# Kernel optimization log

Measured on AMD Instinct MI355X. Metric: run time of the kernel, lower is better.

The kernel has to match this reference:

```python
import jax, jax.numpy as jnp
import numpy as np

N_NODES = 100000
NEG_SLOPE = 0.2


def gat_conv(x, edge_index, W, a_src, a_dst, bias):
    """PyG GATConv, heads=1, concat, add_self_loops=True."""
    N = x.shape[0]
    loop = jnp.arange(N, dtype=edge_index.dtype)
    src = jnp.concatenate([edge_index[0], loop])  # message sources j
    dst = jnp.concatenate([edge_index[1], loop])  # message targets i
    h = x @ W                                      # [N, out]
    asrc = h @ a_src                               # [N]
    adst = h @ a_dst                               # [N]
    e = jax.nn.leaky_relu(asrc[src] + adst[dst], NEG_SLOPE)   # [E+N]
    m = jax.ops.segment_max(e, dst, num_segments=N)           # per-dst max
    w = jnp.exp(e - jax.lax.stop_gradient(m)[dst])
    denom = jax.ops.segment_sum(w, dst, num_segments=N)
    alpha = w / denom[dst]                                     # softmax per dst
    out = jax.ops.segment_sum(alpha[:, None] * h[src], dst, num_segments=N)
    return out + bias


def setup_inputs() -> dict:
    key = jax.random.key(0)
    ks = jax.random.split(key, 16)
    N, E, D = N_NODES, 3200000, 128
    x = jax.random.normal(ks[0], (N, D), dtype=jnp.float32)
    edge_index = jax.random.randint(ks[1], (2, E), 0, N, dtype=jnp.int64)
    def glorot(k, shape):
        fan = sum(shape)
        return jax.random.uniform(k, shape, jnp.float32, -1.0, 1.0) * np.sqrt(6.0 / fan)
    return {
        "x": x,
        "edge_index": edge_index,
        "W1": glorot(ks[2], (D, 16)),
        "a1_src": glorot(ks[3], (16,)),
        "a1_dst": glorot(ks[4], (16,)),
        "b1": jnp.zeros((16,), jnp.float32),
        "W2": glorot(ks[5], (16, 10)),
        "a2_src": glorot(ks[6], (10,)),
        "a2_dst": glorot(ks[7], (10,)),
        "b2": jnp.zeros((10,), jnp.float32),
        "Wl1": glorot(ks[8], (10, 10)),
        "bl1": jnp.zeros((10,), jnp.float32),
        "Wl2": glorot(ks[9], (10, 1)),
        "bl2": jnp.zeros((1,), jnp.float32),
    }


def reference(x, edge_index, W1, a1_src, a1_dst, b1, W2, a2_src, a2_dst, b2,
              Wl1, bl1, Wl2, bl2):
    h = gat_conv(x, edge_index, W1, a1_src, a1_dst, b1)
    h = jax.nn.relu(h)
    h = gat_conv(h, edge_index, W2, a2_src, a2_dst, b2)
    h = h @ Wl1 + bl1
    h = jax.nn.relu(h)
    return h @ Wl2 + bl2  # [N, 1]
```

## Files before the change

### kernel.cpp

```cpp
#include <hip/hip_runtime.h>
#include <hip/hip_fp16.h>


#define NEG 0.2f
#define FSH 7
#define BNODES 128
#define NSBMAX 1024
#define CAPB 4608
#define TILE 4096
#define PES 9

__device__ __forceinline__ float lrelu(float x) { return x > 0.0f ? x : NEG * x; }

__device__ __forceinline__ unsigned fenc(float f) {
    unsigned u = __float_as_uint(f);
    return (u & 0x80000000u) ? ~u : (u | 0x80000000u);
}
__device__ __forceinline__ float fdec(unsigned e) {
    return (e & 0x80000000u) ? __uint_as_float(e & 0x7FFFFFFFu) : __uint_as_float(~e);
}

__device__ __forceinline__ float4 ldh4(const __half* h, size_t off) {
    uint2 u = *(const uint2*)(h + off);
    __half2 a = *(__half2*)&u.x, b = *(__half2*)&u.y;
    float2 fa = __half22float2(a), fb = __half22float2(b);
    return make_float4(fa.x, fa.y, fb.x, fb.y);
}

__global__ __launch_bounds__(256) void k_front(
    const float* __restrict__ x, const float* __restrict__ W1,
    const float* __restrict__ a1s, const float* __restrict__ a1d,
    __half* __restrict__ h1, float* __restrict__ s1, float* __restrict__ d1,
    unsigned* __restrict__ gmax,
    const int* __restrict__ esrc, const int* __restrict__ edst,
    int* __restrict__ bcur, unsigned* __restrict__ pairs,
    int N, int E, int NG, int NC, int NSB)
{
    __shared__ float smem[10500];
    int tid = threadIdx.x;
    int bid = blockIdx.x;
    long long T = (long long)NG + NC;
    int before = (int)(((long long)bid * NC) / T);
    int isc = (int)((((long long)bid + 1) * NC) / T) > before;

    if (isc) {
        unsigned* lsrt = (unsigned*)smem;
        int* lhist = (int*)smem + TILE;
        int* lofs  = lhist + NSBMAX;
        int* gbase = lofs + NSBMAX;
        int* wsum  = gbase + NSBMAX;
        int cid = before;
        int base = cid * TILE;
        int tcnt = min(TILE, E - base);
        for (int i = tid; i < NSB; i += 256) lhist[i] = 0;
        __syncthreads();
        for (int i = tid; i < tcnt; i += 256)
            atomicAdd(&lhist[edst[base + i] >> FSH], 1);
        __syncthreads();
        int i0 = 4 * tid;
        int a0 = (i0 + 0 < NSB) ? lhist[i0 + 0] : 0;
        int a1 = (i0 + 1 < NSB) ? lhist[i0 + 1] : 0;
        int a2 = (i0 + 2 < NSB) ? lhist[i0 + 2] : 0;
        int a3 = (i0 + 3 < NSB) ? lhist[i0 + 3] : 0;
        int s = a0 + a1 + a2 + a3, pfx = s;
#pragma unroll
        for (int off = 1; off < 64; off <<= 1) {
            int t = __shfl_up(pfx, off, 64);
            if ((tid & 63) >= off) pfx += t;
        }
        if ((tid & 63) == 63) wsum[tid >> 6] = pfx;
        __syncthreads();
        int carry = 0;
        for (int w = 0; w < (tid >> 6); ++w) carry += wsum[w];
        int excl = pfx + carry - s;
        if (i0 + 0 < NSB) { lofs[i0 + 0] = excl;                 gbase[i0 + 0] = a0 ? atomicAdd(&bcur[(i0 + 0) * 16], a0) : 0; }
        if (i0 + 1 < NSB) { lofs[i0 + 1] = excl + a0;            gbase[i0 + 1] = a1 ? atomicAdd(&bcur[(i0 + 1) * 16], a1) : 0; }
        if (i0 + 2 < NSB) { lofs[i0 + 2] = excl + a0 + a1;       gbase[i0 + 2] = a2 ? atomicAdd(&bcur[(i0 + 2) * 16], a2) : 0; }
        if (i0 + 3 < NSB) { lofs[i0 + 3] = excl + a0 + a1 + a2;  gbase[i0 + 3] = a3 ? atomicAdd(&bcur[(i0 + 3) * 16], a3) : 0; }
        __syncthreads();
        if (i0 + 0 < NSB) lhist[i0 + 0] = lofs[i0 + 0];
        if (i0 + 1 < NSB) lhist[i0 + 1] = lofs[i0 + 1];
        if (i0 + 2 < NSB) lhist[i0 + 2] = lofs[i0 + 2];
        if (i0 + 3 < NSB) lhist[i0 + 3] = lofs[i0 + 3];
        __syncthreads();
        for (int i = tid; i < tcnt; i += 256) {
            int e = base + i;
            int d = edst[e], srcv = esrc[e];
            int pos = atomicAdd(&lhist[d >> FSH], 1);
            lsrt[pos] = ((unsigned)(d & (BNODES - 1)) << 17) | (unsigned)srcv;
        }
        __syncthreads();
        for (int i = tid; i < tcnt; i += 256) {
            int lo = 0, hi = NSB - 1;
            while (lo < hi) { int mid = (lo + hi + 1) >> 1; if (lofs[mid] <= i) lo = mid; else hi = mid - 1; }
            int rel = gbase[lo] + (i - lofs[lo]);
            if (rel < CAPB) pairs[(size_t)lo * CAPB + rel] = lsrt[i];
        }
        return;
    }

    float* sW = smem;
    float* sx = smem + 2048;
    float* wm = smem + 2048 + 64 * 132;
    int gid = bid - before;
    for (int i = tid; i < 2048; i += 256) sW[i] = W1[i];
    int node0 = gid * 64;
    for (int i = tid; i < 64 * 32; i += 256) {
        int row = i >> 5, c4 = i & 31;
        int n = node0 + row;
        float4 v = make_float4(0.f, 0.f, 0.f, 0.f);
        if (n < N) v = ((const float4*)x)[(size_t)n * 32 + c4];
        *(float4*)&sx[row * 132 + c4 * 4] = v;
    }
    __syncthreads();

    int node = node0 + (tid >> 2);
    int grp  = tid & 3;
    const float* xr = &sx[(tid >> 2) * 132];
    float4 acc = make_float4(0.f, 0.f, 0.f, 0.f);
#pragma unroll 8
    for (int j = 0; j < 128; ++j) {
        float xv = xr[j];
        float4 w = *(const float4*)&sW[j * 16 + grp * 4];
        acc.x += xv * w.x; acc.y += xv * w.y; acc.z += xv * w.z; acc.w += xv * w.w;
    }
    float4 as = ((const float4*)a1s)[grp];
    float4 ad = ((const float4*)a1d)[grp];
    float sv = acc.x * as.x + acc.y * as.y + acc.z * as.z + acc.w * as.w;
    float dv = acc.x * ad.x + acc.y * ad.y + acc.z * ad.z + acc.w * ad.w;
    sv += __shfl_xor(sv, 1); sv += __shfl_xor(sv, 2);
    dv += __shfl_xor(dv, 1); dv += __shfl_xor(dv, 2);
    if (node < N) {
        __half2 p0 = __floats2half2_rn(acc.x, acc.y);
        __half2 p1 = __floats2half2_rn(acc.z, acc.w);
        uint2 u; u.x = *(unsigned*)&p0; u.y = *(unsigned*)&p1;
        *(uint2*)&h1[(size_t)node * 16 + grp * 4] = u;
        if (grp == 0) { s1[node] = sv; d1[node] = dv; }
    }
    float m = (node < N) ? sv : -3.4e38f;
#pragma unroll
    for (int off = 32; off >= 1; off >>= 1) m = fmaxf(m, __shfl_xor(m, off));
    if ((tid & 63) == 0) wm[tid >> 6] = m;
    __syncthreads();
    if (tid == 0) {
        float b = fmaxf(fmaxf(wm[0], wm[1]), fmaxf(wm[2], wm[3]));
        atomicMax(gmax, fenc(b));
    }
}

__global__ __launch_bounds__(512) void k_agg1(
    const int* __restrict__ bcur, const unsigned* __restrict__ pairs,
    const int* __restrict__ esrc, const int* __restrict__ edst,
    const float* __restrict__ s1, const float* __restrict__ d1, const __half* __restrict__ h1,
    const float* __restrict__ b1, const float* __restrict__ W2,
    const float* __restrict__ a2s, const float* __restrict__ a2d,
    __half* __restrict__ h2, float* __restrict__ s2, float* __restrict__ d2,
    const unsigned* __restrict__ gmax1p, unsigned* __restrict__ gmax2, int N, int E)
{
    __shared__ unsigned srt[CAPB];
    __shared__ float accs[BNODES * 17];
    __shared__ int lcnt[BNODES];
    __shared__ int lofs[BNODES + 1];
    __shared__ float dds[BNODES], mbs[BNODES];
    __shared__ float sW[160], sb[16], sas[16], sad[16];
    __shared__ int wsum[8];
    __shared__ float wm[8];

    int tid = threadIdx.x;
    int fb = blockIdx.x;
    if (tid < 160) sW[tid] = W2[tid];
    if (tid < 16) {
        sb[tid]  = b1[tid];
        sas[tid] = (tid < 10) ? a2s[tid] : 0.f;
        sad[tid] = (tid < 10) ? a2d[tid] : 0.f;
    }
    int node0 = fb << FSH;
    float g0 = fdec(*gmax1p);
    if (tid < BNODES) {
        int n = node0 + tid;
        float dd = (n < N) ? d1[n] : 0.f;
        dds[tid] = dd; mbs[tid] = lrelu(g0 + dd);
        lcnt[tid] = 0;
    }
    __syncthreads();

    int rbase = fb * CAPB;
    int cnt = bcur[fb * 16];
    int gg = tid >> 2, q = tid & 3;

    if (cnt <= CAPB) {
        unsigned pe[PES];
#pragma unroll
        for (int u = 0; u < PES; ++u) {
            int i = tid + u * 512;
            bool ok = (i < cnt);
            pe[u] = ok ? pairs[rbase + i] : 0u;
            if (ok) atomicAdd(&lcnt[(pe[u] >> 17) & (BNODES - 1)], 1);
        }
        __syncthreads();
        int c = (tid < BNODES) ? lcnt[tid] : 0;
        int pfx = c;
#pragma unroll
        for (int off = 1; off < 64; off <<= 1) {
            int t = __shfl_up(pfx, off, 64);
            if ((tid & 63) >= off) pfx += t;
        }
        if ((tid & 63) == 63) wsum[tid >> 6] = pfx;
        __syncthreads();
        int carry = 0;
        for (int w = 0; w < (tid >> 6); ++w) carry += wsum[w];
        pfx += carry;
        if (tid < BNODES) { lofs[tid + 1] = pfx; lcnt[tid] = pfx - c; }
        if (tid == 0) lofs[0] = 0;
        __syncthreads();
#pragma unroll
        for (int u = 0; u < PES; ++u) {
            int i = tid + u * 512;
            if (i < cnt) {
                unsigned p = pe[u];
                int pos = atomicAdd(&lcnt[(p >> 17) & (BNODES - 1)], 1);
                srt[pos] = p & 0x1FFFF;
            }
        }
        __syncthreads();

        int n = node0 + gg;
        float4 accv; float den;
        if (n < N) {
            float w = __expf(lrelu(s1[n] + dds[gg]) - mbs[gg]);
            float4 hv = ldh4(h1, (size_t)n * 16 + 4 * q);
            accv = make_float4(w * hv.x, w * hv.y, w * hv.z, w * hv.w);
            den = w;
        } else { accv = make_float4(0.f, 0.f, 0.f, 0.f); den = 0.f; }
        {
            float dd = dds[gg], mb = mbs[gg];
            int j = lofs[gg], j1 = lofs[gg + 1];
            for (; j + 4 <= j1; j += 4) {
                int e0 = srt[j], e1 = srt[j + 1], e2 = srt[j + 2], e3 = srt[j + 3];
                float4 H0 = ldh4(h1, (size_t)e0 * 16 + 4 * q);
                float4 H1 = ldh4(h1, (size_t)e1 * 16 + 4 * q);
                float4 H2 = ldh4(h1, (size_t)e2 * 16 + 4 * q);
                float4 H3 = ldh4(h1, (size_t)e3 * 16 + 4 * q);
                int eq = srt[j + q];
                float wq = __expf(lrelu(s1[eq] + dd) - mb);
                float w0 = __shfl(wq, 0, 4), w1 = __shfl(wq, 1, 4);
                float w2 = __shfl(wq, 2, 4), w3 = __shfl(wq, 3, 4);
                accv.x += w0 * H0.x + w1 * H1.x + w2 * H2.x + w3 * H3.x;
                accv.y += w0 * H0.y + w1 * H1.y + w2 * H2.y + w3 * H3.y;
                accv.z += w0 * H0.z + w1 * H1.z + w2 * H2.z + w3 * H3.z;
                accv.w += w0 * H0.w + w1 * H1.w + w2 * H2.w + w3 * H3.w;
                den += (w0 + w1) + (w2 + w3);
            }
            for (; j < j1; ++j) {
                int e0 = srt[j];
                float w0 = __expf(lrelu(s1[e0] + dd) - mb);
                float4 H0 = ldh4(h1, (size_t)e0 * 16 + 4 * q);
                accv.x += w0 * H0.x; accv.y += w0 * H0.y;
                accv.z += w0 * H0.z; accv.w += w0 * H0.w;
                den += w0;
            }
        }
        accs[gg * 17 + 4 * q + 0] = accv.x;
        accs[gg * 17 + 4 * q + 1] = accv.y;
        accs[gg * 17 + 4 * q + 2] = accv.z;
        accs[gg * 17 + 4 * q + 3] = accv.w;
        if (q == 0) accs[gg * 17 + 16] = den;
        __syncthreads();
    } else {
        for (int i = tid; i < BNODES * 17; i += 512) accs[i] = 0.f;
        __syncthreads();
        if (tid < BNODES) {
            int n = node0 + tid;
            if (n < N) {
                float w = __expf(lrelu(s1[n] + dds[tid]) - mbs[tid]);
#pragma unroll
                for (int t = 0; t < 16; ++t)
                    accs[tid * 17 + t] = w * __half2float(h1[(size_t)n * 16 + t]);
                accs[tid * 17 + 16] = w;
            }
        }
        __syncthreads();
        for (int i = tid; i < E; i += 512) {
            int d = edst[i];
            if ((d >> FSH) != fb) continue;
            int nl = d & (BNODES - 1), src = esrc[i];
            float w = __expf(lrelu(s1[src] + dds[nl]) - mbs[nl]);
#pragma unroll
            for (int t = 0; t < 16; ++t)
                atomicAdd(&accs[nl * 17 + t], w * __half2float(h1[(size_t)src * 16 + t]));
            atomicAdd(&accs[nl * 17 + 16], w);
        }
        __syncthreads();
    }

    int g = tid >> 4, k = tid & 15;
    float sval = -3.4e38f;
#pragma unroll
    for (int qq = 0; qq < 4; ++qq) {
        int nl = g * 4 + qq, nn = node0 + nl;
        if (nn >= N) continue;
        float inv = 1.f / accs[nl * 17 + 16];
        float o = fmaxf(accs[nl * 17 + k] * inv + sb[k], 0.f);
        float hh = 0.f;
#pragma unroll
        for (int kk = 0; kk < 16; ++kk) {
            float ov = __shfl(o, kk, 16);
            if (k < 10) hh += ov * sW[kk * 10 + k];
        }
        if (k >= 10) hh = 0.f;
        float ts = hh * sas[k];
        float td = hh * sad[k];
#pragma unroll
        for (int off = 1; off < 16; off <<= 1) {
            ts += __shfl_xor(ts, off, 16);
            td += __shfl_xor(td, off, 16);
        }
        h2[(size_t)nn * 16 + k] = __float2half_rn(hh);
        if (k == 0) { s2[nn] = ts; d2[nn] = td; }
        sval = fmaxf(sval, ts);
    }
    float m = sval;
#pragma unroll
    for (int off = 32; off >= 1; off >>= 1) m = fmaxf(m, __shfl_xor(m, off));
    if ((tid & 63) == 0) wm[tid >> 6] = m;
    __syncthreads();
    if (tid == 0) {
        float bmx = wm[0];
#pragma unroll
        for (int i = 1; i < 8; ++i) bmx = fmaxf(bmx, wm[i]);
        atomicMax(gmax2, fenc(bmx));
    }
}

__global__ __launch_bounds__(512) void k_agg2(
    const int* __restrict__ bcur, const unsigned* __restrict__ pairs,
    const int* __restrict__ esrc, const int* __restrict__ edst,
    const float* __restrict__ s2, const float* __restrict__ d2, const __half* __restrict__ h2,
    const float* __restrict__ b2, const float* __restrict__ Wl1, const float* __restrict__ bl1,
    const float* __restrict__ Wl2, const float* __restrict__ bl2,
    const unsigned* __restrict__ gmax2p, float* __restrict__ out, int N, int E)
{
    __shared__ unsigned srt[CAPB];
    __shared__ float accs[BNODES * 17];
    __shared__ int lcnt[BNODES];
    __shared__ int lofs[BNODES + 1];
    __shared__ float dds[BNODES], mbs[BNODES];
    __shared__ float sW1[100], sb1[16], sW2[16], sb2g[16];
    __shared__ float sbl2;
    __shared__ int wsum[8];

    int tid = threadIdx.x;
    int fb = blockIdx.x;
    if (tid < 100) sW1[tid] = Wl1[tid];
    if (tid < 16) {
        sb1[tid]  = (tid < 10) ? bl1[tid] : 0.f;
        sW2[tid]  = (tid < 10) ? Wl2[tid] : 0.f;
        sb2g[tid] = (tid < 10) ? b2[tid]  : 0.f;
    }
    if (tid == 0) sbl2 = bl2[0];
    int node0 = fb << FSH;
    float g0 = fdec(*gmax2p);
    if (tid < BNODES) {
        int n = node0 + tid;
        float dd = (n < N) ? d2[n] : 0.f;
        dds[tid] = dd; mbs[tid] = lrelu(g0 + dd);
        lcnt[tid] = 0;
    }
    __syncthreads();

    int rbase = fb * CAPB;
    int cnt = bcur[fb * 16];
    int gg = tid >> 2, q = tid & 3;

    if (cnt <= CAPB) {
        unsigned pe[PES];
#pragma unroll
        for (int u = 0; u < PES; ++u) {
            int i = tid + u * 512;
            bool ok = (i < cnt);
            pe[u] = ok ? pairs[rbase + i] : 0u;
            if (ok) atomicAdd(&lcnt[(pe[u] >> 17) & (BNODES - 1)], 1);
        }
        __syncthreads();
        int c = (tid < BNODES) ? lcnt[tid] : 0;
        int pfx = c;
#pragma unroll
        for (int off = 1; off < 64; off <<= 1) {
            int t = __shfl_up(pfx, off, 64);
            if ((tid & 63) >= off) pfx += t;
        }
        if ((tid & 63) == 63) wsum[tid >> 6] = pfx;
        __syncthreads();
        int carry = 0;
        for (int w = 0; w < (tid >> 6); ++w) carry += wsum[w];
        pfx += carry;
        if (tid < BNODES) { lofs[tid + 1] = pfx; lcnt[tid] = pfx - c; }
        if (tid == 0) lofs[0] = 0;
        __syncthreads();
#pragma unroll
        for (int u = 0; u < PES; ++u) {
            int i = tid + u * 512;
            if (i < cnt) {
                unsigned p = pe[u];
                int pos = atomicAdd(&lcnt[(p >> 17) & (BNODES - 1)], 1);
                srt[pos] = p & 0x1FFFF;
            }
        }
        __syncthreads();

        int n = node0 + gg;
        float4 accv; float den;
        if (n < N) {
            float w = __expf(lrelu(s2[n] + dds[gg]) - mbs[gg]);
            float4 hv = ldh4(h2, (size_t)n * 16 + 4 * q);
            accv = make_float4(w * hv.x, w * hv.y, w * hv.z, w * hv.w);
            den = w;
        } else { accv = make_float4(0.f, 0.f, 0.f, 0.f); den = 0.f; }
        {
            float dd = dds[gg], mb = mbs[gg];
            int j = lofs[gg], j1 = lofs[gg + 1];
            for (; j + 4 <= j1; j += 4) {
                int e0 = srt[j], e1 = srt[j + 1], e2 = srt[j + 2], e3 = srt[j + 3];
                float4 H0 = ldh4(h2, (size_t)e0 * 16 + 4 * q);
                float4 H1 = ldh4(h2, (size_t)e1 * 16 + 4 * q);
                float4 H2 = ldh4(h2, (size_t)e2 * 16 + 4 * q);
                float4 H3 = ldh4(h2, (size_t)e3 * 16 + 4 * q);
                int eq = srt[j + q];
                float wq = __expf(lrelu(s2[eq] + dd) - mb);
                float w0 = __shfl(wq, 0, 4), w1 = __shfl(wq, 1, 4);
                float w2 = __shfl(wq, 2, 4), w3 = __shfl(wq, 3, 4);
                accv.x += w0 * H0.x + w1 * H1.x + w2 * H2.x + w3 * H3.x;
                accv.y += w0 * H0.y + w1 * H1.y + w2 * H2.y + w3 * H3.y;
                accv.z += w0 * H0.z + w1 * H1.z + w2 * H2.z + w3 * H3.z;
                accv.w += w0 * H0.w + w1 * H1.w + w2 * H2.w + w3 * H3.w;
                den += (w0 + w1) + (w2 + w3);
            }
            for (; j < j1; ++j) {
                int e0 = srt[j];
                float w0 = __expf(lrelu(s2[e0] + dd) - mb);
                float4 H0 = ldh4(h2, (size_t)e0 * 16 + 4 * q);
                accv.x += w0 * H0.x; accv.y += w0 * H0.y;
                accv.z += w0 * H0.z; accv.w += w0 * H0.w;
                den += w0;
            }
        }
        accs[gg * 17 + 4 * q + 0] = accv.x;
        accs[gg * 17 + 4 * q + 1] = accv.y;
        accs[gg * 17 + 4 * q + 2] = accv.z;
        accs[gg * 17 + 4 * q + 3] = accv.w;
        if (q == 0) accs[gg * 17 + 16] = den;
        __syncthreads();
    } else {
        for (int i = tid; i < BNODES * 17; i += 512) accs[i] = 0.f;
        __syncthreads();
        if (tid < BNODES) {
            int n = node0 + tid;
            if (n < N) {
                float w = __expf(lrelu(s2[n] + dds[tid]) - mbs[tid]);
#pragma unroll
                for (int t = 0; t < 16; ++t)
                    accs[tid * 17 + t] = w * __half2float(h2[(size_t)n * 16 + t]);
                accs[tid * 17 + 16] = w;
            }
        }
        __syncthreads();
        for (int i = tid; i < E; i += 512) {
            int d = edst[i];
            if ((d >> FSH) != fb) continue;
            int nl = d & (BNODES - 1), src = esrc[i];
            float w = __expf(lrelu(s2[src] + dds[nl]) - mbs[nl]);
#pragma unroll
            for (int t = 0; t < 16; ++t)
                atomicAdd(&accs[nl * 17 + t], w * __half2float(h2[(size_t)src * 16 + t]));
            atomicAdd(&accs[nl * 17 + 16], w);
        }
        __syncthreads();
    }

    int g = tid >> 4, k = tid & 15;
    bool fk = k < 10;
#pragma unroll
    for (int qq = 0; qq < 4; ++qq) {
        int nl = g * 4 + qq, nn = node0 + nl;
        if (nn >= N) continue;
        float inv = 1.f / accs[nl * 17 + 16];
        float o = fk ? accs[nl * 17 + k] * inv + sb2g[k] : 0.f;
        float v = sb1[k];
#pragma unroll
        for (int kk = 0; kk < 10; ++kk) {
            float ov = __shfl(o, kk, 16);
            if (fk) v += ov * sW1[kk * 10 + k];
        }
        float t = fmaxf(v, 0.f);
        float cc = t * sW2[k];
#pragma unroll
        for (int off = 1; off < 16; off <<= 1) cc += __shfl_xor(cc, off, 16);
        if (k == 0) out[nn] = cc + sbl2;
    }
}

extern "C" void kernel_launch(void* const* d_in, const int* in_sizes, int n_in,
                              void* d_out, int out_size, void* d_ws, size_t ws_size,
                              hipStream_t stream)
{
    const float* x   = (const float*)d_in[0];
    const int*   ei  = (const int*)  d_in[1];
    const float* W1  = (const float*)d_in[2];
    const float* a1s = (const float*)d_in[3];
    const float* a1d = (const float*)d_in[4];
    const float* b1  = (const float*)d_in[5];
    const float* W2  = (const float*)d_in[6];
    const float* a2s = (const float*)d_in[7];
    const float* a2d = (const float*)d_in[8];
    const float* b2  = (const float*)d_in[9];
    const float* Wl1 = (const float*)d_in[10];
    const float* bl1 = (const float*)d_in[11];
    const float* Wl2 = (const float*)d_in[12];
    const float* bl2 = (const float*)d_in[13];

    int N = in_sizes[0] / 128;
    int E = in_sizes[1] / 2;
    const int* ei_src = ei;
    const int* ei_dst = ei + E;
    int NSB = (N + BNODES - 1) >> FSH;

    size_t Np = ((size_t)N + 3) & ~(size_t)3;
    size_t need_bytes = (16 + (size_t)NSB * 16) * 4 + Np * 20 * 4 + (size_t)NSB * CAPB * 4;
    if (ws_size < need_bytes) return;

    unsigned* gmax1 = (unsigned*)d_ws;
    unsigned* gmax2 = gmax1 + 1;
    int* bcur = (int*)d_ws + 16;
    float* rest = (float*)d_ws + 16 + (size_t)NSB * 16;
    __half* h1 = (__half*)rest;
    float* s1 = rest + Np * 8;
    float* d1 = s1 + Np;
    __half* h2 = (__half*)(d1 + Np);
    float* s2 = (float*)(h2) + Np * 8;
    float* d2 = s2 + Np;
    unsigned* pairs = (unsigned*)(d2 + Np);

    int NG = (N + 63) / 64;
    int NC = (E + TILE - 1) / TILE;

    hipMemsetAsync(d_ws, 0, (16 + (size_t)NSB * 16) * sizeof(int), stream);
    hipLaunchKernelGGL(k_front, dim3(NG + NC), dim3(256), 0, stream,
                       x, W1, a1s, a1d, h1, s1, d1, gmax1,
                       ei_src, ei_dst, bcur, pairs, N, E, NG, NC, NSB);
    hipLaunchKernelGGL(k_agg1, dim3(NSB), dim3(512), 0, stream,
                       bcur, pairs, ei_src, ei_dst, s1, d1, h1, b1, W2, a2s, a2d,
                       h2, s2, d2, gmax1, gmax2, N, E);
    hipLaunchKernelGGL(k_agg2, dim3(NSB), dim3(512), 0, stream,
                       bcur, pairs, ei_src, ei_dst, s2, d2, h2, b2, Wl1, bl1, Wl2, bl2,
                       gmax2, (float*)d_out, N, E);
}
```

Before: 279.1 us.

## Split per-node edge lists across lane pairs with 16-byte feature gathers

The four lanes per destination node are regrouped into two pairs. Each pair handles half of the node's edge list, and each lane gathers 8 half-precision features with one 16-byte load instead of 4 with an 8-byte load. The partial sums are combined with xor shuffles. Separately, the edge tile size in the front kernel is doubled, which enlarges its shared memory buffer. The aim is fewer, wider gather instructions and more parallelism within each node's edge list. The cost is extra shuffle reductions, more registers per lane, and more shared memory in the front kernel.

```diff
diff --git a/kernel.cpp b/kernel.cpp
--- a/kernel.cpp
+++ b/kernel.cpp
@@ -7,7 +7,7 @@
 #define BNODES 128
 #define NSBMAX 1024
 #define CAPB 4608
-#define TILE 4096
+#define TILE 8192
 #define PES 9
 
 __device__ __forceinline__ float lrelu(float x) { return x > 0.0f ? x : NEG * x; }
@@ -25,6 +25,16 @@
     __half2 a = *(__half2*)&u.x, b = *(__half2*)&u.y;
     float2 fa = __half22float2(a), fb = __half22float2(b);
     return make_float4(fa.x, fa.y, fb.x, fb.y);
+}
+
+__device__ __forceinline__ void ldh8(const __half* h, size_t off, float4& a, float4& b) {
+    uint4 u = *(const uint4*)(h + off);
+    __half2 p0 = *(__half2*)&u.x, p1 = *(__half2*)&u.y;
+    __half2 p2 = *(__half2*)&u.z, p3 = *(__half2*)&u.w;
+    float2 f0 = __half22float2(p0), f1 = __half22float2(p1);
+    float2 f2 = __half22float2(p2), f3 = __half22float2(p3);
+    a = make_float4(f0.x, f0.y, f1.x, f1.y);
+    b = make_float4(f2.x, f2.y, f3.x, f3.y);
 }
 
 __global__ __launch_bounds__(256) void k_front(
@@ -36,7 +46,7 @@
     int* __restrict__ bcur, unsigned* __restrict__ pairs,
     int N, int E, int NG, int NC, int NSB)
 {
-    __shared__ float smem[10500];
+    __shared__ float smem[11268];
     int tid = threadIdx.x;
     int bid = blockIdx.x;
     long long T = (long long)NG + NC;
@@ -225,46 +235,67 @@
         __syncthreads();
 
         int n = node0 + gg;
-        float4 accv; float den;
-        if (n < N) {
-            float w = __expf(lrelu(s1[n] + dds[gg]) - mbs[gg]);
-            float4 hv = ldh4(h1, (size_t)n * 16 + 4 * q);
-            accv = make_float4(w * hv.x, w * hv.y, w * hv.z, w * hv.w);
+        int sub = q >> 1, ql = q & 1;
+        float dd = dds[gg], mb = mbs[gg];
+        float4 aA = make_float4(0.f, 0.f, 0.f, 0.f);
+        float4 aB = make_float4(0.f, 0.f, 0.f, 0.f);
+        float den = 0.f;
+        if (n < N && sub == 0) {
+            float w = __expf(lrelu(s1[n] + dd) - mb);
+            float4 hA, hB; ldh8(h1, (size_t)n * 16 + 8 * ql, hA, hB);
+            aA = make_float4(w * hA.x, w * hA.y, w * hA.z, w * hA.w);
+            aB = make_float4(w * hB.x, w * hB.y, w * hB.z, w * hB.w);
             den = w;
-        } else { accv = make_float4(0.f, 0.f, 0.f, 0.f); den = 0.f; }
+        }
         {
-            float dd = dds[gg], mb = mbs[gg];
-            int j = lofs[gg], j1 = lofs[gg + 1];
+            int lo = lofs[gg], hi = lofs[gg + 1];
+            int half = (hi - lo + 1) >> 1;
+            int j  = lo + sub * half;
+            int j1 = sub ? hi : lo + half;
             for (; j + 4 <= j1; j += 4) {
                 int e0 = srt[j], e1 = srt[j + 1], e2 = srt[j + 2], e3 = srt[j + 3];
-                float4 H0 = ldh4(h1, (size_t)e0 * 16 + 4 * q);
-                float4 H1 = ldh4(h1, (size_t)e1 * 16 + 4 * q);
-                float4 H2 = ldh4(h1, (size_t)e2 * 16 + 4 * q);
-                float4 H3 = ldh4(h1, (size_t)e3 * 16 + 4 * q);
-                int eq = srt[j + q];
-                float wq = __expf(lrelu(s1[eq] + dd) - mb);
-                float w0 = __shfl(wq, 0, 4), w1 = __shfl(wq, 1, 4);
-                float w2 = __shfl(wq, 2, 4), w3 = __shfl(wq, 3, 4);
-                accv.x += w0 * H0.x + w1 * H1.x + w2 * H2.x + w3 * H3.x;
-                accv.y += w0 * H0.y + w1 * H1.y + w2 * H2.y + w3 * H3.y;
-                accv.z += w0 * H0.z + w1 * H1.z + w2 * H2.z + w3 * H3.z;
-                accv.w += w0 * H0.w + w1 * H1.w + w2 * H2.w + w3 * H3.w;
+                int eA = ql ? e1 : e0, eB = ql ? e3 : e2;
+                float wqA = __expf(lrelu(s1[eA] + dd) - mb);
+                float wqB = __expf(lrelu(s1[eB] + dd) - mb);
+                float w0 = __shfl(wqA, 0, 2), w1 = __shfl(wqA, 1, 2);
+                float w2 = __shfl(wqB, 0, 2), w3 = __shfl(wqB, 1, 2);
+                float4 H0a, H0b, H1a, H1b, H2a, H2b, H3a, H3b;
+                ldh8(h1, (size_t)e0 * 16 + 8 * ql, H0a, H0b);
+                ldh8(h1, (size_t)e1 * 16 + 8 * ql, H1a, H1b);
+                ldh8(h1, (size_t)e2 * 16 + 8 * ql, H2a, H2b);
+                ldh8(h1, (size_t)e3 * 16 + 8 * ql, H3a, H3b);
+                aA.x += w0 * H0a.x + w1 * H1a.x + w2 * H2a.x + w3 * H3a.x;
+                aA.y += w0 * H0a.y + w1 * H1a.y + w2 * H2a.y + w3 * H3a.y;
+                aA.z += w0 * H0a.z + w1 * H1a.z + w2 * H2a.z + w3 * H3a.z;
+                aA.w += w0 * H0a.w + w1 * H1a.w + w2 * H2a.w + w3 * H3a.w;
+                aB.x += w0 * H0b.x + w1 * H1b.x + w2 * H2b.x + w3 * H3b.x;
+                aB.y += w0 * H0b.y + w1 * H1b.y + w2 * H2b.y + w3 * H3b.y;
+                aB.z += w0 * H0b.z + w1 * H1b.z + w2 * H2b.z + w3 * H3b.z;
+                aB.w += w0 * H0b.w + w1 * H1b.w + w2 * H2b.w + w3 * H3b.w;
                 den += (w0 + w1) + (w2 + w3);
             }
             for (; j < j1; ++j) {
                 int e0 = srt[j];
                 float w0 = __expf(lrelu(s1[e0] + dd) - mb);
-                float4 H0 = ldh4(h1, (size_t)e0 * 16 + 4 * q);
-                accv.x += w0 * H0.x; accv.y += w0 * H0.y;
-                accv.z += w0 * H0.z; accv.w += w0 * H0.w;
+                float4 Ha, Hb; ldh8(h1, (size_t)e0 * 16 + 8 * ql, Ha, Hb);
+                aA.x += w0 * Ha.x; aA.y += w0 * Ha.y; aA.z += w0 * Ha.z; aA.w += w0 * Ha.w;
+                aB.x += w0 * Hb.x; aB.y += w0 * Hb.y; aB.z += w0 * Hb.z; aB.w += w0 * Hb.w;
                 den += w0;
             }
         }
-        accs[gg * 17 + 4 * q + 0] = accv.x;
-        accs[gg * 17 + 4 * q + 1] = accv.y;
-        accs[gg * 17 + 4 * q + 2] = accv.z;
-        accs[gg * 17 + 4 * q + 3] = accv.w;
-        if (q == 0) accs[gg * 17 + 16] = den;
+        aA.x += __shfl_xor(aA.x, 2, 4); aA.y += __shfl_xor(aA.y, 2, 4);
+        aA.z += __shfl_xor(aA.z, 2, 4); aA.w += __shfl_xor(aA.w, 2, 4);
+        aB.x += __shfl_xor(aB.x, 2, 4); aB.y += __shfl_xor(aB.y, 2, 4);
+        aB.z += __shfl_xor(aB.z, 2, 4); aB.w += __shfl_xor(aB.w, 2, 4);
+        den  += __shfl_xor(den, 2, 4);
+        if (sub == 0) {
+            int cbase = gg * 17 + 8 * ql;
+            accs[cbase + 0] = aA.x; accs[cbase + 1] = aA.y;
+            accs[cbase + 2] = aA.z; accs[cbase + 3] = aA.w;
+            accs[cbase + 4] = aB.x; accs[cbase + 5] = aB.y;
+            accs[cbase + 6] = aB.z; accs[cbase + 7] = aB.w;
+            if (q == 0) accs[gg * 17 + 16] = den;
+        }
         __syncthreads();
     } else {
         for (int i = tid; i < BNODES * 17; i += 512) accs[i] = 0.f;
@@ -409,46 +440,67 @@
         __syncthreads();
 
         int n = node0 + gg;
-        float4 accv; float den;
-        if (n < N) {
-            float w = __expf(lrelu(s2[n] + dds[gg]) - mbs[gg]);
-            float4 hv = ldh4(h2, (size_t)n * 16 + 4 * q);
-            accv = make_float4(w * hv.x, w * hv.y, w * hv.z, w * hv.w);
+        int sub = q >> 1, ql = q & 1;
+        float dd = dds[gg], mb = mbs[gg];
+        float4 aA = make_float4(0.f, 0.f, 0.f, 0.f);
+        float4 aB = make_float4(0.f, 0.f, 0.f, 0.f);
+        float den = 0.f;
+        if (n < N && sub == 0) {
+            float w = __expf(lrelu(s2[n] + dd) - mb);
+            float4 hA, hB; ldh8(h2, (size_t)n * 16 + 8 * ql, hA, hB);
+            aA = make_float4(w * hA.x, w * hA.y, w * hA.z, w * hA.w);
+            aB = make_float4(w * hB.x, w * hB.y, w * hB.z, w * hB.w);
             den = w;
-        } else { accv = make_float4(0.f, 0.f, 0.f, 0.f); den = 0.f; }
+        }
         {
-            float dd = dds[gg], mb = mbs[gg];
-            int j = lofs[gg], j1 = lofs[gg + 1];
+            int lo = lofs[gg], hi = lofs[gg + 1];
+            int half = (hi - lo + 1) >> 1;
+            int j  = lo + sub * half;
+            int j1 = sub ? hi : lo + half;
             for (; j + 4 <= j1; j += 4) {
                 int e0 = srt[j], e1 = srt[j + 1], e2 = srt[j + 2], e3 = srt[j + 3];
-                float4 H0 = ldh4(h2, (size_t)e0 * 16 + 4 * q);
-                float4 H1 = ldh4(h2, (size_t)e1 * 16 + 4 * q);
-                float4 H2 = ldh4(h2, (size_t)e2 * 16 + 4 * q);
-                float4 H3 = ldh4(h2, (size_t)e3 * 16 + 4 * q);
-                int eq = srt[j + q];
-                float wq = __expf(lrelu(s2[eq] + dd) - mb);
-                float w0 = __shfl(wq, 0, 4), w1 = __shfl(wq, 1, 4);
-                float w2 = __shfl(wq, 2, 4), w3 = __shfl(wq, 3, 4);
-                accv.x += w0 * H0.x + w1 * H1.x + w2 * H2.x + w3 * H3.x;
-                accv.y += w0 * H0.y + w1 * H1.y + w2 * H2.y + w3 * H3.y;
-                accv.z += w0 * H0.z + w1 * H1.z + w2 * H2.z + w3 * H3.z;
-                accv.w += w0 * H0.w + w1 * H1.w + w2 * H2.w + w3 * H3.w;
+                int eA = ql ? e1 : e0, eB = ql ? e3 : e2;
+                float wqA = __expf(lrelu(s2[eA] + dd) - mb);
+                float wqB = __expf(lrelu(s2[eB] + dd) - mb);
+                float w0 = __shfl(wqA, 0, 2), w1 = __shfl(wqA, 1, 2);
+                float w2 = __shfl(wqB, 0, 2), w3 = __shfl(wqB, 1, 2);
+                float4 H0a, H0b, H1a, H1b, H2a, H2b, H3a, H3b;
+                ldh8(h2, (size_t)e0 * 16 + 8 * ql, H0a, H0b);
+                ldh8(h2, (size_t)e1 * 16 + 8 * ql, H1a, H1b);
+                ldh8(h2, (size_t)e2 * 16 + 8 * ql, H2a, H2b);
+                ldh8(h2, (size_t)e3 * 16 + 8 * ql, H3a, H3b);
+                aA.x += w0 * H0a.x + w1 * H1a.x + w2 * H2a.x + w3 * H3a.x;
+                aA.y += w0 * H0a.y + w1 * H1a.y + w2 * H2a.y + w3 * H3a.y;
+                aA.z += w0 * H0a.z + w1 * H1a.z + w2 * H2a.z + w3 * H3a.z;
+                aA.w += w0 * H0a.w + w1 * H1a.w + w2 * H2a.w + w3 * H3a.w;
+                aB.x += w0 * H0b.x + w1 * H1b.x + w2 * H2b.x + w3 * H3b.x;
+                aB.y += w0 * H0b.y + w1 * H1b.y + w2 * H2b.y + w3 * H3b.y;
+                aB.z += w0 * H0b.z + w1 * H1b.z + w2 * H2b.z + w3 * H3b.z;
+                aB.w += w0 * H0b.w + w1 * H1b.w + w2 * H2b.w + w3 * H3b.w;
                 den += (w0 + w1) + (w2 + w3);
             }
             for (; j < j1; ++j) {
                 int e0 = srt[j];
                 float w0 = __expf(lrelu(s2[e0] + dd) - mb);
-                float4 H0 = ldh4(h2, (size_t)e0 * 16 + 4 * q);
-                accv.x += w0 * H0.x; accv.y += w0 * H0.y;
-                accv.z += w0 * H0.z; accv.w += w0 * H0.w;
+                float4 Ha, Hb; ldh8(h2, (size_t)e0 * 16 + 8 * ql, Ha, Hb);
+                aA.x += w0 * Ha.x; aA.y += w0 * Ha.y; aA.z += w0 * Ha.z; aA.w += w0 * Ha.w;
+                aB.x += w0 * Hb.x; aB.y += w0 * Hb.y; aB.z += w0 * Hb.z; aB.w += w0 * Hb.w;
                 den += w0;
             }
         }
-        accs[gg * 17 + 4 * q + 0] = accv.x;
-        accs[gg * 17 + 4 * q + 1] = accv.y;
-        accs[gg * 17 + 4 * q + 2] = accv.z;
-        accs[gg * 17 + 4 * q + 3] = accv.w;
-        if (q == 0) accs[gg * 17 + 16] = den;
+        aA.x += __shfl_xor(aA.x, 2, 4); aA.y += __shfl_xor(aA.y, 2, 4);
+        aA.z += __shfl_xor(aA.z, 2, 4); aA.w += __shfl_xor(aA.w, 2, 4);
+        aB.x += __shfl_xor(aB.x, 2, 4); aB.y += __shfl_xor(aB.y, 2, 4);
+        aB.z += __shfl_xor(aB.z, 2, 4); aB.w += __shfl_xor(aB.w, 2, 4);
+        den  += __shfl_xor(den, 2, 4);
+        if (sub == 0) {
+            int cbase = gg * 17 + 8 * ql;
+            accs[cbase + 0] = aA.x; accs[cbase + 1] = aA.y;
+            accs[cbase + 2] = aA.z; accs[cbase + 3] = aA.w;
+            accs[cbase + 4] = aB.x; accs[cbase + 5] = aB.y;
+            accs[cbase + 6] = aB.z; accs[cbase + 7] = aB.w;
+            if (q == 0) accs[gg * 17 + 16] = den;
+        }
         __syncthreads();
     } else {
         for (int i = tid; i < BNODES * 17; i += 512) accs[i] = 0.f;
```

New measurement: 285.6 us. +2.3%, slower.

## Split aggregation buckets across two half-node blocks and register-tile front GEMM

Applied to the files above, without the earlier changes.

The aggregation kernels now launch two 256-thread blocks per 128-node bucket. Each block reads the whole bucket's edge list but keeps only the edges for its 64 destination nodes, which shrinks shared memory and raises occupancy and block count. The cost is that every edge pair in a bucket is now read twice. The front kernel also drops the shared-memory staging of x and keeps each thread's 32-column slice in registers, with a 16-wide accumulator reduced by shuffles, using a padded W layout to avoid bank conflicts. This adds register pressure, and a new fallback path triggers when a half-bucket overflows its shared capacity.

```diff
diff --git a/kernel.cpp b/kernel.cpp
--- a/kernel.cpp
+++ b/kernel.cpp
@@ -8,7 +8,9 @@
 #define NSBMAX 1024
 #define CAPB 4608
 #define TILE 4096
-#define PES 9
+#define HN 64
+#define SCAP 3072
+#define PESA 18
 
 __device__ __forceinline__ float lrelu(float x) { return x > 0.0f ? x : NEG * x; }
 
@@ -36,7 +38,7 @@
     int* __restrict__ bcur, unsigned* __restrict__ pairs,
     int N, int E, int NG, int NC, int NSB)
 {
-    __shared__ float smem[10500];
+    __shared__ float smem[7172];
     int tid = threadIdx.x;
     int bid = blockIdx.x;
     long long T = (long long)NG + NC;
@@ -100,44 +102,69 @@
     }
 
     float* sW = smem;
-    float* sx = smem + 2048;
-    float* wm = smem + 2048 + 64 * 132;
+    float* wm = smem + 2060;
     int gid = bid - before;
-    for (int i = tid; i < 2048; i += 256) sW[i] = W1[i];
+    for (int i = tid; i < 2048; i += 256) sW[i + ((i >> 9) << 2)] = W1[i];
     int node0 = gid * 64;
-    for (int i = tid; i < 64 * 32; i += 256) {
-        int row = i >> 5, c4 = i & 31;
-        int n = node0 + row;
-        float4 v = make_float4(0.f, 0.f, 0.f, 0.f);
-        if (n < N) v = ((const float4*)x)[(size_t)n * 32 + c4];
-        *(float4*)&sx[row * 132 + c4 * 4] = v;
+    int node = node0 + (tid >> 2);
+    int q = tid & 3;
+    bool valid = node < N;
+    float4 xr[8];
+    {
+        const float4* xp = (const float4*)x + (size_t)node * 32 + q * 8;
+#pragma unroll
+        for (int k = 0; k < 8; ++k)
+            xr[k] = valid ? xp[k] : make_float4(0.f, 0.f, 0.f, 0.f);
     }
     __syncthreads();
 
-    int node = node0 + (tid >> 2);
-    int grp  = tid & 3;
-    const float* xr = &sx[(tid >> 2) * 132];
-    float4 acc = make_float4(0.f, 0.f, 0.f, 0.f);
-#pragma unroll 8
-    for (int j = 0; j < 128; ++j) {
-        float xv = xr[j];
-        float4 w = *(const float4*)&sW[j * 16 + grp * 4];
-        acc.x += xv * w.x; acc.y += xv * w.y; acc.z += xv * w.z; acc.w += xv * w.w;
-    }
-    float4 as = ((const float4*)a1s)[grp];
-    float4 ad = ((const float4*)a1d)[grp];
-    float sv = acc.x * as.x + acc.y * as.y + acc.z * as.z + acc.w * as.w;
-    float dv = acc.x * ad.x + acc.y * ad.y + acc.z * ad.z + acc.w * ad.w;
-    sv += __shfl_xor(sv, 1); sv += __shfl_xor(sv, 2);
-    dv += __shfl_xor(dv, 1); dv += __shfl_xor(dv, 2);
-    if (node < N) {
-        __half2 p0 = __floats2half2_rn(acc.x, acc.y);
-        __half2 p1 = __floats2half2_rn(acc.z, acc.w);
+    float acc[16];
+#pragma unroll
+    for (int c = 0; c < 16; ++c) acc[c] = 0.f;
+    int wbase = q * 516;
+#pragma unroll
+    for (int k = 0; k < 8; ++k) {
+        float xs0 = xr[k].x, xs1 = xr[k].y, xs2 = xr[k].z, xs3 = xr[k].w;
+#pragma unroll
+        for (int t = 0; t < 4; ++t) {
+            float xv = (t == 0) ? xs0 : (t == 1) ? xs1 : (t == 2) ? xs2 : xs3;
+            const float4* wrow = (const float4*)&sW[wbase + (k * 4 + t) * 16];
+            float4 w0 = wrow[0], w1 = wrow[1], w2 = wrow[2], w3 = wrow[3];
+            acc[0]  += xv * w0.x; acc[1]  += xv * w0.y; acc[2]  += xv * w0.z; acc[3]  += xv * w0.w;
+            acc[4]  += xv * w1.x; acc[5]  += xv * w1.y; acc[6]  += xv * w1.z; acc[7]  += xv * w1.w;
+            acc[8]  += xv * w2.x; acc[9]  += xv * w2.y; acc[10] += xv * w2.z; acc[11] += xv * w2.w;
+            acc[12] += xv * w3.x; acc[13] += xv * w3.y; acc[14] += xv * w3.z; acc[15] += xv * w3.w;
+        }
+    }
+#pragma unroll
+    for (int c = 0; c < 16; ++c) {
+        acc[c] += __shfl_xor(acc[c], 1);
+        acc[c] += __shfl_xor(acc[c], 2);
+    }
+    float sv = 0.f, dv = 0.f;
+    {
+        const float4* asp = (const float4*)a1s;
+        const float4* adp = (const float4*)a1d;
+#pragma unroll
+        for (int r = 0; r < 4; ++r) {
+            float4 as = asp[r], ad = adp[r];
+            sv += acc[r*4+0]*as.x + acc[r*4+1]*as.y + acc[r*4+2]*as.z + acc[r*4+3]*as.w;
+            dv += acc[r*4+0]*ad.x + acc[r*4+1]*ad.y + acc[r*4+2]*ad.z + acc[r*4+3]*ad.w;
+        }
+    }
+    if (valid) {
+        float4 av;
+        if      (q == 0) av = make_float4(acc[0],  acc[1],  acc[2],  acc[3]);
+        else if (q == 1) av = make_float4(acc[4],  acc[5],  acc[6],  acc[7]);
+        else if (q == 2) av = make_float4(acc[8],  acc[9],  acc[10], acc[11]);
+        else             av = make_float4(acc[12], acc[13], acc[14], acc[15]);
+        __half2 p0 = __floats2half2_rn(av.x, av.y);
+        __half2 p1 = __floats2half2_rn(av.z, av.w);
         uint2 u; u.x = *(unsigned*)&p0; u.y = *(unsigned*)&p1;
-        *(uint2*)&h1[(size_t)node * 16 + grp * 4] = u;
-        if (grp == 0) { s1[node] = sv; d1[node] = dv; }
-    }
-    float m = (node < N) ? sv : -3.4e38f;
+        *(uint2*)&h1[(size_t)node * 16 + q * 4] = u;
+        if (q == 0) { s1[node] = sv; d1[node] = dv; }
+    }
+    float m = valid ? sv : -3.4e38f;
 #pragma unroll
     for (int off = 32; off >= 1; off >>= 1) m = fmaxf(m, __shfl_xor(m, off));
     if ((tid & 63) == 0) wm[tid >> 6] = m;
@@ -148,7 +175,7 @@
     }
 }
 
-__global__ __launch_bounds__(512) void k_agg1(
+__global__ __launch_bounds__(256) void k_agg1(
     const int* __restrict__ bcur, const unsigned* __restrict__ pairs,
     const int* __restrict__ esrc, const int* __restrict__ edst,
     const float* __restrict__ s1, const float* __restrict__ d1, const __half* __restrict__ h1,
@@ -157,26 +184,26 @@
     __half* __restrict__ h2, float* __restrict__ s2, float* __restrict__ d2,
     const unsigned* __restrict__ gmax1p, unsigned* __restrict__ gmax2, int N, int E)
 {
-    __shared__ unsigned srt[CAPB];
-    __shared__ float accs[BNODES * 17];
-    __shared__ int lcnt[BNODES];
-    __shared__ int lofs[BNODES + 1];
-    __shared__ float dds[BNODES], mbs[BNODES];
+    __shared__ unsigned srt[SCAP];
+    __shared__ float accs[HN * 17];
+    __shared__ int lcnt[HN];
+    __shared__ int lofs[HN + 1];
+    __shared__ float dds[HN], mbs[HN];
     __shared__ float sW[160], sb[16], sas[16], sad[16];
-    __shared__ int wsum[8];
-    __shared__ float wm[8];
+    __shared__ float wm[4];
 
     int tid = threadIdx.x;
-    int fb = blockIdx.x;
+    int fb = blockIdx.x >> 1;
+    int hf = blockIdx.x & 1;
+    int node0 = blockIdx.x << 6;
     if (tid < 160) sW[tid] = W2[tid];
     if (tid < 16) {
         sb[tid]  = b1[tid];
         sas[tid] = (tid < 10) ? a2s[tid] : 0.f;
         sad[tid] = (tid < 10) ? a2d[tid] : 0.f;
     }
-    int node0 = fb << FSH;
     float g0 = fdec(*gmax1p);
-    if (tid < BNODES) {
+    if (tid < HN) {
         int n = node0 + tid;
         float dd = (n < N) ? d1[n] : 0.f;
         dds[tid] = dd; mbs[tid] = lrelu(g0 + dd);
@@ -188,38 +215,47 @@
     int cnt = bcur[fb * 16];
     int gg = tid >> 2, q = tid & 3;
 
-    if (cnt <= CAPB) {
-        unsigned pe[PES];
-#pragma unroll
-        for (int u = 0; u < PES; ++u) {
-            int i = tid + u * 512;
-            bool ok = (i < cnt);
-            pe[u] = ok ? pairs[rbase + i] : 0u;
-            if (ok) atomicAdd(&lcnt[(pe[u] >> 17) & (BNODES - 1)], 1);
-        }
-        __syncthreads();
-        int c = (tid < BNODES) ? lcnt[tid] : 0;
-        int pfx = c;
-#pragma unroll
-        for (int off = 1; off < 64; off <<= 1) {
-            int t = __shfl_up(pfx, off, 64);
-            if ((tid & 63) >= off) pfx += t;
-        }
-        if ((tid & 63) == 63) wsum[tid >> 6] = pfx;
-        __syncthreads();
-        int carry = 0;
-        for (int w = 0; w < (tid >> 6); ++w) carry += wsum[w];
-        pfx += carry;
-        if (tid < BNODES) { lofs[tid + 1] = pfx; lcnt[tid] = pfx - c; }
-        if (tid == 0) lofs[0] = 0;
-        __syncthreads();
-#pragma unroll
-        for (int u = 0; u < PES; ++u) {
-            int i = tid + u * 512;
+    bool ok = (cnt <= CAPB);
+    unsigned pe[PESA];
+    if (ok) {
+#pragma unroll
+        for (int u = 0; u < PESA; ++u) {
+            int i = tid + u * 256;
+            bool v = (i < cnt);
+            pe[u] = v ? pairs[rbase + i] : 0u;
+            if (v) {
+                int dl = (pe[u] >> 17) & (BNODES - 1);
+                if ((dl >> 6) == hf) atomicAdd(&lcnt[dl & (HN - 1)], 1);
+            }
+        }
+        __syncthreads();
+        if (tid < HN) {
+            int c = lcnt[tid];
+            int pfx = c;
+#pragma unroll
+            for (int off = 1; off < 64; off <<= 1) {
+                int t = __shfl_up(pfx, off, 64);
+                if (tid >= off) pfx += t;
+            }
+            lofs[tid + 1] = pfx;
+            lcnt[tid] = pfx - c;
+            if (tid == 0) lofs[0] = 0;
+        }
+        __syncthreads();
+        if (lofs[HN] > SCAP) ok = false;
+    }
+
+    if (ok) {
+#pragma unroll
+        for (int u = 0; u < PESA; ++u) {
+            int i = tid + u * 256;
             if (i < cnt) {
                 unsigned p = pe[u];
-                int pos = atomicAdd(&lcnt[(p >> 17) & (BNODES - 1)], 1);
-                srt[pos] = p & 0x1FFFF;
+                int dl = (p >> 17) & (BNODES - 1);
+                if ((dl >> 6) == hf) {
+                    int pos = atomicAdd(&lcnt[dl & (HN - 1)], 1);
+                    srt[pos] = p & 0x1FFFF;
+                }
             }
         }
         __syncthreads();
@@ -267,9 +303,9 @@
         if (q == 0) accs[gg * 17 + 16] = den;
         __syncthreads();
     } else {
-        for (int i = tid; i < BNODES * 17; i += 512) accs[i] = 0.f;
-        __syncthreads();
-        if (tid < BNODES) {
+        for (int i = tid; i < HN * 17; i += 256) accs[i] = 0.f;
+        __syncthreads();
+        if (tid < HN) {
             int n = node0 + tid;
             if (n < N) {
                 float w = __expf(lrelu(s1[n] + dds[tid]) - mbs[tid]);
@@ -280,10 +316,10 @@
             }
         }
         __syncthreads();
-        for (int i = tid; i < E; i += 512) {
+        for (int i = tid; i < E; i += 256) {
             int d = edst[i];
-            if ((d >> FSH) != fb) continue;
-            int nl = d & (BNODES - 1), src = esrc[i];
+            if ((d >> 6) != blockIdx.x) continue;
+            int nl = d & (HN - 1), src = esrc[i];
             float w = __expf(lrelu(s1[src] + dds[nl]) - mbs[nl]);
 #pragma unroll
             for (int t = 0; t < 16; ++t)
@@ -325,14 +361,12 @@
     if ((tid & 63) == 0) wm[tid >> 6] = m;
     __syncthreads();
     if (tid == 0) {
-        float bmx = wm[0];
-#pragma unroll
-        for (int i = 1; i < 8; ++i) bmx = fmaxf(bmx, wm[i]);
+        float bmx = fmaxf(fmaxf(wm[0], wm[1]), fmaxf(wm[2], wm[3]));
         atomicMax(gmax2, fenc(bmx));
     }
 }
 
-__global__ __launch_bounds__(512) void k_agg2(
+__global__ __launch_bounds__(256) void k_agg2(
     const int* __restrict__ bcur, const unsigned* __restrict__ pairs,
     const int* __restrict__ esrc, const int* __restrict__ edst,
     const float* __restrict__ s2, const float* __restrict__ d2, const __half* __restrict__ h2,
@@ -340,17 +374,18 @@
     const float* __restrict__ Wl2, const float* __restrict__ bl2,
     const unsigned* __restrict__ gmax2p, float* __restrict__ out, int N, int E)
 {
-    __shared__ unsigned srt[CAPB];
-    __shared__ float accs[BNODES * 17];
-    __shared__ int lcnt[BNODES];
-    __shared__ int lofs[BNODES + 1];
-    __shared__ float dds[BNODES], mbs[BNODES];
+    __shared__ unsigned srt[SCAP];
+    __shared__ float accs[HN * 17];
+    __shared__ int lcnt[HN];
+    __shared__ int lofs[HN + 1];
+    __shared__ float dds[HN], mbs[HN];
     __shared__ float sW1[100], sb1[16], sW2[16], sb2g[16];
     __shared__ float sbl2;
-    __shared__ int wsum[8];
 
     int tid = threadIdx.x;
-    int fb = blockIdx.x;
+    int fb = blockIdx.x >> 1;
+    int hf = blockIdx.x & 1;
+    int node0 = blockIdx.x << 6;
     if (tid < 100) sW1[tid] = Wl1[tid];
     if (tid < 16) {
         sb1[tid]  = (tid < 10) ? bl1[tid] : 0.f;
@@ -358,9 +393,8 @@
         sb2g[tid] = (tid < 10) ? b2[tid]  : 0.f;
     }
     if (tid == 0) sbl2 = bl2[0];
-    int node0 = fb << FSH;
     float g0 = fdec(*gmax2p);
-    if (tid < BNODES) {
+    if (tid < HN) {
         int n = node0 + tid;
         float dd = (n < N) ? d2[n] : 0.f;
         dds[tid] = dd; mbs[tid] = lrelu(g0 + dd);
@@ -372,38 +406,47 @@
     int cnt = bcur[fb * 16];
     int gg = tid >> 2, q = tid & 3;
 
-    if (cnt <= CAPB) {
-        unsigned pe[PES];
-#pragma unroll
-        for (int u = 0; u < PES; ++u) {
-            int i = tid + u * 512;
-            bool ok = (i < cnt);
-            pe[u] = ok ? pairs[rbase + i] : 0u;
-            if (ok) atomicAdd(&lcnt[(pe[u] >> 17) & (BNODES - 1)], 1);
-        }
-        __syncthreads();
-        int c = (tid < BNODES) ? lcnt[tid] : 0;
-        int pfx = c;
-#pragma unroll
-        for (int off = 1; off < 64; off <<= 1) {
-            int t = __shfl_up(pfx, off, 64);
-            if ((tid & 63) >= off) pfx += t;
-        }
-        if ((tid & 63) == 63) wsum[tid >> 6] = pfx;
-        __syncthreads();
-        int carry = 0;
-        for (int w = 0; w < (tid >> 6); ++w) carry += wsum[w];
-        pfx += carry;
-        if (tid < BNODES) { lofs[tid + 1] = pfx; lcnt[tid] = pfx - c; }
-        if (tid == 0) lofs[0] = 0;
-        __syncthreads();
-#pragma unroll
-        for (int u = 0; u < PES; ++u) {
-            int i = tid + u * 512;
+    bool ok = (cnt <= CAPB);
+    unsigned pe[PESA];
+    if (ok) {
+#pragma unroll
+        for (int u = 0; u < PESA; ++u) {
+            int i = tid + u * 256;
+            bool v = (i < cnt);
+            pe[u] = v ? pairs[rbase + i] : 0u;
+            if (v) {
+                int dl = (pe[u] >> 17) & (BNODES - 1);
+                if ((dl >> 6) == hf) atomicAdd(&lcnt[dl & (HN - 1)], 1);
+            }
+        }
+        __syncthreads();
+        if (tid < HN) {
+            int c = lcnt[tid];
+            int pfx = c;
+#pragma unroll
+            for (int off = 1; off < 64; off <<= 1) {
+                int t = __shfl_up(pfx, off, 64);
+                if (tid >= off) pfx += t;
+            }
+            lofs[tid + 1] = pfx;
+            lcnt[tid] = pfx - c;
+            if (tid == 0) lofs[0] = 0;
+        }
+        __syncthreads();
+        if (lofs[HN] > SCAP) ok = false;
+    }
+
+    if (ok) {
+#pragma unroll
+        for (int u = 0; u < PESA; ++u) {
+            int i = tid + u * 256;
             if (i < cnt) {
                 unsigned p = pe[u];
-                int pos = atomicAdd(&lcnt[(p >> 17) & (BNODES - 1)], 1);
-                srt[pos] = p & 0x1FFFF;
+                int dl = (p >> 17) & (BNODES - 1);
+                if ((dl >> 6) == hf) {
+                    int pos = atomicAdd(&lcnt[dl & (HN - 1)], 1);
+                    srt[pos] = p & 0x1FFFF;
+                }
             }
         }
         __syncthreads();
@@ -451,9 +494,9 @@
         if (q == 0) accs[gg * 17 + 16] = den;
         __syncthreads();
     } else {
-        for (int i = tid; i < BNODES * 17; i += 512) accs[i] = 0.f;
-        __syncthreads();
-        if (tid < BNODES) {
+        for (int i = tid; i < HN * 17; i += 256) accs[i] = 0.f;
+        __syncthreads();
+        if (tid < HN) {
             int n = node0 + tid;
             if (n < N) {
                 float w = __expf(lrelu(s2[n] + dds[tid]) - mbs[tid]);
@@ -464,10 +507,10 @@
             }
         }
         __syncthreads();
-        for (int i = tid; i < E; i += 512) {
+        for (int i = tid; i < E; i += 256) {
             int d = edst[i];
-            if ((d >> FSH) != fb) continue;
-            int nl = d & (BNODES - 1), src = esrc[i];
+            if ((d >> 6) != blockIdx.x) continue;
+            int nl = d & (HN - 1), src = esrc[i];
             float w = __expf(lrelu(s2[src] + dds[nl]) - mbs[nl]);
 #pragma unroll
             for (int t = 0; t < 16; ++t)
@@ -547,10 +590,10 @@
     hipLaunchKernelGGL(k_front, dim3(NG + NC), dim3(256), 0, stream,
                        x, W1, a1s, a1d, h1, s1, d1, gmax1,
                        ei_src, ei_dst, bcur, pairs, N, E, NG, NC, NSB);
-    hipLaunchKernelGGL(k_agg1, dim3(NSB), dim3(512), 0, stream,
+    hipLaunchKernelGGL(k_agg1, dim3(NSB * 2), dim3(256), 0, stream,
                        bcur, pairs, ei_src, ei_dst, s1, d1, h1, b1, W2, a2s, a2d,
                        h2, s2, d2, gmax1, gmax2, N, E);
-    hipLaunchKernelGGL(k_agg2, dim3(NSB), dim3(512), 0, stream,
+    hipLaunchKernelGGL(k_agg2, dim3(NSB * 2), dim3(256), 0, stream,
                        bcur, pairs, ei_src, ei_dst, s2, d2, h2, b2, Wl1, bl1, Wl2, bl2,
                        gmax2, (float*)d_out, N, E);
 }
```

Result: no change. 280.6 us (+0.5%).
